# Optimization experiments

Measured on AMD Instinct MI355X. Metric: run time of the kernel, lower is better.

Reference implementation:

```python
import jax, jax.numpy as jnp
import numpy as np

N_NODES = 100000
N_EDGES = 1600000
D_IN = 512
D_HID = 128
N_CLASSES = 100


def _gcn_norm(edge_index, n_nodes):
    # Add self loops and compute symmetric normalization D^{-1/2} (A+I) D^{-1/2}
    sl = jnp.arange(n_nodes, dtype=edge_index.dtype)
    src = jnp.concatenate([edge_index[0], sl])
    dst = jnp.concatenate([edge_index[1], sl])
    deg = jax.ops.segment_sum(jnp.ones_like(dst, dtype=jnp.float32), dst,
                              num_segments=n_nodes)
    dinv = jnp.where(deg > 0, jax.lax.rsqrt(deg), 0.0)
    norm = dinv[src] * dinv[dst]  # [E + N]
    return src, dst, norm


def _gcn_layer(x, W, b, src, dst, norm, n_nodes):
    h = x @ W                                  # [N, d_out] (transform first, like PyG GCNConv)
    msg = h[src] * norm[:, None]               # [E+N, d_out] gather + scale
    out = jax.ops.segment_sum(msg, dst, num_segments=n_nodes)  # scatter-add
    return out + b


def setup_inputs() -> dict:
    key = jax.random.key(0)
    ks = jax.random.split(key, 6)
    x = jax.random.normal(ks[0], (N_NODES, D_IN), dtype=jnp.float32)
    edge_index = jax.random.randint(ks[1], (2, N_EDGES), 0, N_NODES, dtype=jnp.int64)
    W1 = jax.random.normal(ks[2], (D_IN, D_HID), dtype=jnp.float32) * (1.0 / np.sqrt(D_IN))
    b1 = jnp.zeros((D_HID,), dtype=jnp.float32)
    W2 = jax.random.normal(ks[3], (D_HID, N_CLASSES), dtype=jnp.float32) * (1.0 / np.sqrt(D_HID))
    b2 = jnp.zeros((N_CLASSES,), dtype=jnp.float32)
    return {"x": x, "edge_index": edge_index, "W1": W1, "b1": b1, "W2": W2, "b2": b2}


def reference(x, edge_index, W1, b1, W2, b2):
    n_nodes = x.shape[0]
    src, dst, norm = _gcn_norm(edge_index, n_nodes)
    h = jax.nn.relu(_gcn_layer(x, W1, b1, src, dst, norm, n_nodes))
    logits = _gcn_layer(h, W2, b2, src, dst, norm, n_nodes)
    return jax.nn.log_softmax(logits, axis=-1)
```

## Files before the change

### kernel.cpp

```cpp
#include <hip/hip_runtime.h>
#include <math.h>

typedef __attribute__((ext_vector_type(8))) short short8;
typedef __attribute__((ext_vector_type(4))) float f32x4;
typedef _Float16 half8 __attribute__((ext_vector_type(8)));
typedef __fp16 fp16x2 __attribute__((ext_vector_type(2)));
typedef unsigned int uint;

__device__ inline uint f2bf(float f) {
    uint u = __float_as_uint(f);
    return (u + 0x7fffu + ((u >> 16) & 1u)) >> 16;
}
__device__ inline uint pack2(float lo, float hi) { return f2bf(lo) | (f2bf(hi) << 16); }
__device__ inline float bflo(uint u) { return __uint_as_float(u << 16); }
__device__ inline float bfhi(uint u) { return __uint_as_float(u & 0xffff0000u); }
__device__ inline uint cvtpk(float lo, float hi) {
    uint r;
    asm("v_cvt_pk_bf16_f32 %0, %1, %2" : "=v"(r) : "v"(lo), "v"(hi));
    return r;
}
__device__ inline uint pkh(float lo, float hi) {
    union { fp16x2 h; uint u; } c;
    c.h = __builtin_amdgcn_cvt_pkrtz(lo, hi);
    return c.u;
}
__device__ inline void gload16(const void* g, void* l) {
    __builtin_amdgcn_global_load_lds(
        (const __attribute__((address_space(1))) void*)g,
        (__attribute__((address_space(3))) void*)l, 16, 0, 0);
}

__global__ void k_prep(const int* __restrict__ dst, int E, int nbE, int* __restrict__ cnt,
                       const float* __restrict__ W1, ushort* __restrict__ w1frag,
                       const float* __restrict__ W2, const float* __restrict__ b2,
                       ushort* __restrict__ w2frag, float* __restrict__ b2pad) {
    int bid = blockIdx.x;
    if (bid < nbE) {
        int i = bid * 256 + threadIdx.x;
        if (i < E) atomicAdd(&cnt[dst[i]], 1);
        return;
    }
    bid -= nbE;
    if (bid < 32) {
        int tid = bid * 256 + threadIdx.x;
        int ks = tid >> 9;
        int t = (tid >> 6) & 7;
        int l = tid & 63;
        int kbase = ks * 32 + (l >> 4) * 8;
        int c = t * 16 + (l & 15);
#pragma unroll
        for (int j = 0; j < 8; j++) {
            float v = W1[(size_t)(kbase + j) * 128 + c];
            union { _Float16 h; ushort u; } cv;
            cv.h = (_Float16)v;
            w1frag[(size_t)tid * 8 + j] = cv.u;
        }
        return;
    }
    bid -= 32;
    {
        int tid = bid * 256 + threadIdx.x;
        if (tid < 1792) {
            int q = tid / 448;
            int t = (tid >> 6) % 7;
            int l = tid & 63;
            int kbase = q * 32 + (l >> 4) * 8;
            int c = t * 16 + (l & 15);
#pragma unroll
            for (int j = 0; j < 8; j++) {
                float v = (c < 100) ? W2[(kbase + j) * 100 + c] : 0.f;
                w2frag[(size_t)tid * 8 + j] = (ushort)f2bf(v);
            }
        } else if (tid < 1792 + 112) {
            int c = tid - 1792;
            b2pad[c] = (c < 100) ? b2[c] : -1e30f;
        }
    }
}

__global__ __launch_bounds__(512) void k_scan1(const int* __restrict__ cnt, int* __restrict__ rp,
                                               int* __restrict__ partials, float* __restrict__ dinv,
                                               int N) {
    __shared__ int s[512];
    int i = blockIdx.x * 512 + threadIdx.x;
    int v = (i < N) ? cnt[i] : 0;
    if (i < N) dinv[i] = rsqrtf((float)(v + 1));
    s[threadIdx.x] = v;
    __syncthreads();
    for (int d = 1; d < 512; d <<= 1) {
        int t = (threadIdx.x >= d) ? s[threadIdx.x - d] : 0;
        __syncthreads();
        s[threadIdx.x] += t;
        __syncthreads();
    }
    if (i < N) rp[i] = s[threadIdx.x] - v;
    if (threadIdx.x == 511) partials[blockIdx.x] = s[511];
}

__global__ __launch_bounds__(256) void k_scan2(int* __restrict__ partials, int nb) {
    __shared__ int s[256];
    int carry = 0;
    for (int base = 0; base < nb; base += 256) {
        int i = base + threadIdx.x;
        int v = (i < nb) ? partials[i] : 0;
        s[threadIdx.x] = v;
        __syncthreads();
        for (int d = 1; d < 256; d <<= 1) {
            int t = (threadIdx.x >= d) ? s[threadIdx.x - d] : 0;
            __syncthreads();
            s[threadIdx.x] += t;
            __syncthreads();
        }
        if (i < nb) partials[i] = carry + s[threadIdx.x] - v;
        carry += s[255];
        __syncthreads();
    }
}

__global__ __launch_bounds__(512) void k_scan3(int* __restrict__ rp, const int* __restrict__ partials,
                                               int N, int E) {
    int i = blockIdx.x * 512 + threadIdx.x;
    if (i < N) rp[i] += partials[blockIdx.x];
    if (i == 0) rp[N] = E;
}

__global__ void k_fill(const int* __restrict__ src, const int* __restrict__ dst, int E,
                       const int* __restrict__ rp, int* __restrict__ cursor,
                       const float* __restrict__ dinv, float2* __restrict__ colw) {
    int i = blockIdx.x * 256 + threadIdx.x;
    if (i < E) {
        int d = dst[i];
        int s = src[i];
        int pos = rp[d] + atomicAdd(&cursor[d], 1);
        colw[pos] = make_float2(__int_as_float(s), dinv[s]);
    }
}

__global__ __launch_bounds__(256) void k_gemm1(const float* __restrict__ x,
                                               const uint4* __restrict__ w1f,
                                               uint* __restrict__ h1, int N) {
    __shared__ __align__(16) char lds[40960];
    int tid = threadIdx.x, wv = tid >> 6, l = tid & 63;
    int cl = l & 15, kg = l >> 4;
    int row0 = blockIdx.x * 32;
    int rhalf = wv & 1, chalf = wv >> 1;

    int xr = tid >> 3, xs = tid & 7;
    int xrg = row0 + xr; if (xrg >= N) xrg = N - 1;
    const float* xsrc = x + (size_t)xrg * 512 + xs * 8;

    auto stageB = [&](int c) {
        char* bbase = lds + 8192 + (c & 1) * 16384;
        const char* bsrc = (const char*)w1f + (size_t)c * 16384;
#pragma unroll
        for (int i = 0; i < 4; i++) {
            int s = i * 256 + tid;
            gload16(bsrc + (size_t)s * 16, bbase + (size_t)(s - l) * 16);
        }
    };

    float4 f0, f1;
    auto loadx = [&](int c) {
        const float* p = xsrc + c * 64;
        f0 = *(const float4*)p;
        f1 = *(const float4*)(p + 4);
    };
    auto writex = [&](int c) {
        char* xb = lds + (c & 1) * 4096;
        uint4 v;
        v.x = pkh(f0.x, f0.y);
        v.y = pkh(f0.z, f0.w);
        v.z = pkh(f1.x, f1.y);
        v.w = pkh(f1.z, f1.w);
        *(uint4*)(xb + xr * 128 + ((xs ^ (xr & 7)) * 16)) = v;
    };

    f32x4 acc[4];
#pragma unroll
    for (int t = 0; t < 4; t++) acc[t] = (f32x4){0.f, 0.f, 0.f, 0.f};

    union U { uint4 u4; half8 h8; };
    int arow = rhalf * 16 + cl;

    loadx(0);
    stageB(0);
    writex(0);
    __syncthreads();

    for (int c = 0; c < 8; c++) {
        if (c < 7) { loadx(c + 1); stageB(c + 1); }
        const char* xb = lds + (c & 1) * 4096;
        const char* bb = lds + 8192 + (c & 1) * 16384;
#pragma unroll
        for (int k2 = 0; k2 < 2; k2++) {
            U A;
            A.u4 = *(const uint4*)(xb + arow * 128 + (((k2 * 4 + kg) ^ (arow & 7)) * 16));
#pragma unroll
            for (int tt = 0; tt < 4; tt++) {
                U B;
                B.u4 = *(const uint4*)(bb + (size_t)(((k2 * 8 + chalf * 4 + tt) * 64 + l)) * 16);
                acc[tt] = __builtin_amdgcn_mfma_f32_16x16x32_f16(A.h8, B.h8, acc[tt], 0, 0, 0);
            }
        }
        if (c < 7) writex(c + 1);
        __syncthreads();
    }

    uint* hsp = (uint*)lds + (size_t)wv * (16 * 33);
#pragma unroll
    for (int tt = 0; tt < 4; tt++)
#pragma unroll
        for (int r = 0; r < 4; r++) {
            float mine = acc[tt][r];
            float other = __shfl_xor(mine, 1, 64);
            if ((cl & 1) == 0)
                hsp[(kg * 4 + r) * 33 + tt * 8 + (cl >> 1)] = cvtpk(mine, other);
        }
#pragma unroll
    for (int p = 0; p < 8; p++) {
        int it = p * 2 + (l >> 5);
        int gr = row0 + rhalf * 16 + it;
        if (gr < N) h1[(size_t)gr * 64 + chalf * 32 + (l & 31)] = hsp[it * 33 + (l & 31)];
    }
}

template <bool RELU_BIAS>
__global__ __launch_bounds__(256) void k_agg(const uint* __restrict__ h, const float* __restrict__ dinv,
                                             const int* __restrict__ rp, const float2* __restrict__ colw,
                                             const float* __restrict__ bias, uint* __restrict__ outb, int N) {
    int wave = threadIdx.x >> 6, lane = threadIdx.x & 63;
    int v = blockIdx.x * 4 + wave;
    if (v >= N) return;
    float dv = dinv[v];
    float wself = dv * dv;
    uint us = h[(size_t)v * 64 + lane];
    float acc0 = bflo(us) * wself;
    float acc1 = bfhi(us) * wself;
    int e0 = rp[v], e1 = rp[v + 1];
    int i = e0;
    for (; i + 8 <= e1; i += 8) {
        float2 q[8];
        uint u[8];
#pragma unroll
        for (int j = 0; j < 8; j++) q[j] = colw[i + j];
#pragma unroll
        for (int j = 0; j < 8; j++) u[j] = h[(size_t)__float_as_int(q[j].x) * 64 + lane];
#pragma unroll
        for (int j = 0; j < 8; j++) {
            float w = q[j].y * dv;
            acc0 = fmaf(bflo(u[j]), w, acc0);
            acc1 = fmaf(bfhi(u[j]), w, acc1);
        }
    }
    if (i + 4 <= e1) {
        float2 q[4];
        uint u[4];
#pragma unroll
        for (int j = 0; j < 4; j++) q[j] = colw[i + j];
#pragma unroll
        for (int j = 0; j < 4; j++) u[j] = h[(size_t)__float_as_int(q[j].x) * 64 + lane];
#pragma unroll
        for (int j = 0; j < 4; j++) {
            float w = q[j].y * dv;
            acc0 = fmaf(bflo(u[j]), w, acc0);
            acc1 = fmaf(bfhi(u[j]), w, acc1);
        }
        i += 4;
    }
    for (; i < e1; i++) {
        float2 q = colw[i];
        uint u = h[(size_t)__float_as_int(q.x) * 64 + lane];
        float w = q.y * dv;
        acc0 = fmaf(bflo(u), w, acc0);
        acc1 = fmaf(bfhi(u), w, acc1);
    }
    if (RELU_BIAS) {
        float2 b = *(const float2*)&bias[2 * lane];
        acc0 = fmaxf(acc0 + b.x, 0.f);
        acc1 = fmaxf(acc1 + b.y, 0.f);
    }
    outb[(size_t)v * 64 + lane] = pack2(acc0, acc1);
}

__global__ __launch_bounds__(256) void k_out_mfma(const uint* __restrict__ g2u,
                                                  const uint4* __restrict__ w2fragG,
                                                  const float* __restrict__ b2pad,
                                                  float* __restrict__ out, int N) {
    __shared__ uint4 w2s[1792];
    __shared__ float b2s[112];
    int tid = threadIdx.x;
    for (int i = tid; i < 1792; i += 256) w2s[i] = w2fragG[i];
    if (tid < 112) b2s[tid] = b2pad[tid];
    __syncthreads();

    int w = tid >> 6, l = tid & 63;
    int v0 = blockIdx.x * 128 + w * 32;
    int cl = l & 15, gq = l >> 4;

    f32x4 acc[2][7];
#pragma unroll
    for (int m = 0; m < 2; m++)
#pragma unroll
        for (int t = 0; t < 7; t++) acc[m][t] = (f32x4){0.f, 0.f, 0.f, 0.f};

    union U { uint4 u4; short8 s8; };

#pragma unroll
    for (int q = 0; q < 4; q++) {
        short8 afr[2];
#pragma unroll
        for (int m = 0; m < 2; m++) {
            int rv = v0 + m * 16 + cl;
            if (rv >= N) rv = N - 1;
            U a;
            a.u4 = *(const uint4*)&g2u[(size_t)rv * 64 + q * 16 + gq * 4];
            afr[m] = a.s8;
        }
#pragma unroll
        for (int t = 0; t < 7; t++) {
            U b;
            b.u4 = w2s[(q * 7 + t) * 64 + l];
            acc[0][t] = __builtin_amdgcn_mfma_f32_16x16x32_bf16(afr[0], b.s8, acc[0][t], 0, 0, 0);
            acc[1][t] = __builtin_amdgcn_mfma_f32_16x16x32_bf16(afr[1], b.s8, acc[1][t], 0, 0, 0);
        }
    }

    float bsv[7];
#pragma unroll
    for (int t = 0; t < 7; t++) bsv[t] = b2s[t * 16 + cl];

#pragma unroll
    for (int m = 0; m < 2; m++) {
#pragma unroll
        for (int r = 0; r < 4; r++) {
            int row = v0 + m * 16 + gq * 4 + r;
            float lg[7];
#pragma unroll
            for (int t = 0; t < 7; t++) lg[t] = acc[m][t][r] + bsv[t];
            float mx = lg[0];
#pragma unroll
            for (int t = 1; t < 7; t++) mx = fmaxf(mx, lg[t]);
            mx = fmaxf(mx, __shfl_xor(mx, 1, 64));
            mx = fmaxf(mx, __shfl_xor(mx, 2, 64));
            mx = fmaxf(mx, __shfl_xor(mx, 4, 64));
            mx = fmaxf(mx, __shfl_xor(mx, 8, 64));
            float s = 0.f;
#pragma unroll
            for (int t = 0; t < 7; t++) s += __expf(lg[t] - mx);
            s += __shfl_xor(s, 1, 64);
            s += __shfl_xor(s, 2, 64);
            s += __shfl_xor(s, 4, 64);
            s += __shfl_xor(s, 8, 64);
            float lse = mx + __logf(s);
            if (row < N) {
#pragma unroll
                for (int t = 0; t < 7; t++) {
                    int c = t * 16 + cl;
                    if (c < 100) out[(size_t)row * 100 + c] = lg[t] - lse;
                }
            }
        }
    }
}

extern "C" void kernel_launch(void* const* d_in, const int* in_sizes, int n_in,
                              void* d_out, int out_size, void* d_ws, size_t ws_size,
                              hipStream_t stream) {
    const float* x  = (const float*)d_in[0];
    const int*   ei = (const int*)d_in[1];
    const float* W1 = (const float*)d_in[2];
    const float* b1 = (const float*)d_in[3];
    const float* W2 = (const float*)d_in[4];
    const float* b2 = (const float*)d_in[5];
    float* out = (float*)d_out;

    int N = in_sizes[0] / 512;
    int E = in_sizes[1] / 2;
    const int* srcI = ei;
    const int* dstI = ei + E;

    char* wsb = (char*)d_ws;
    size_t off = 0;
    auto alloc = [&](size_t bytes) {
        void* p = wsb + off;
        off = (off + bytes + 255) & ~(size_t)255;
        return p;
    };
    int*    cnt      = (int*)alloc((size_t)N * 4);
    int*    cursor   = (int*)alloc((size_t)N * 4);
    float*  dinv     = (float*)alloc((size_t)N * 4);
    int*    rp       = (int*)alloc((size_t)(N + 1) * 4);
    int*    partials = (int*)alloc(1024 * 4);
    ushort* w1f      = (ushort*)alloc(8192 * 8 * 2);
    ushort* w2frag   = (ushort*)alloc(1792 * 8 * 2);
    float*  b2pad    = (float*)alloc(112 * 4);
    float2* colw     = (float2*)alloc((size_t)E * 8);
    uint*   h1       = (uint*)alloc((size_t)N * 64 * 4);
    uint*   a1       = (uint*)alloc((size_t)N * 64 * 4);
    uint*   g2       = h1;

    hipMemsetAsync(cnt, 0, (size_t)2 * (((size_t)N * 4 + 255) & ~(size_t)255), stream);

    int nbE = (E + 255) / 256;
    k_prep<<<nbE + 40, 256, 0, stream>>>(dstI, E, nbE, cnt, W1, w1f, W2, b2, w2frag, b2pad);
    int nb = (N + 511) / 512;
    k_scan1<<<nb, 512, 0, stream>>>(cnt, rp, partials, dinv, N);
    k_scan2<<<1, 256, 0, stream>>>(partials, nb);
    k_scan3<<<nb, 512, 0, stream>>>(rp, partials, N, E);
    k_fill<<<(E + 255) / 256, 256, 0, stream>>>(srcI, dstI, E, rp, cursor, dinv, colw);

    k_gemm1<<<(N + 31) / 32, 256, 0, stream>>>(x, (const uint4*)w1f, h1, N);
    k_agg<true><<<(N + 3) / 4, 256, 0, stream>>>(h1, dinv, rp, colw, b1, a1, N);
    k_agg<false><<<(N + 3) / 4, 256, 0, stream>>>(a1, dinv, rp, colw, nullptr, g2, N);
    k_out_mfma<<<(N + 127) / 128, 256, 0, stream>>>(g2, (const uint4*)w2frag, b2pad, out, N);
}
```

Baseline: 378.6 us.

## Fuse CSR build into one cooperative kernel and widen GEMM1 blocks

Replaces the memset, prep, three scan kernels and fill kernel with a single cooperative kernel that uses grid-wide syncs between the zeroing, count, scan, offset and fill phases. This removes several launch gaps and the memset. The GEMM1 kernel now uses 512-thread blocks covering 64 rows, so each staged W1 chunk is shared by more rows. The cost is grid.sync overhead, a fixed 1024-block grid doing strided loops, and larger LDS use per block, which may lower occupancy.

```diff
diff --git a/kernel.cpp b/kernel.cpp
--- a/kernel.cpp
+++ b/kernel.cpp
@@ -1,5 +1,8 @@
 #include <hip/hip_runtime.h>
+#include <hip/hip_cooperative_groups.h>
 #include <math.h>
+
+namespace cg = cooperative_groups;
 
 typedef __attribute__((ext_vector_type(8))) short short8;
 typedef __attribute__((ext_vector_type(4))) float f32x4;
@@ -30,131 +33,127 @@
         (__attribute__((address_space(3))) void*)l, 16, 0, 0);
 }
 
-__global__ void k_prep(const int* __restrict__ dst, int E, int nbE, int* __restrict__ cnt,
-                       const float* __restrict__ W1, ushort* __restrict__ w1frag,
-                       const float* __restrict__ W2, const float* __restrict__ b2,
-                       ushort* __restrict__ w2frag, float* __restrict__ b2pad) {
-    int bid = blockIdx.x;
-    if (bid < nbE) {
-        int i = bid * 256 + threadIdx.x;
-        if (i < E) atomicAdd(&cnt[dst[i]], 1);
-        return;
-    }
-    bid -= nbE;
-    if (bid < 32) {
-        int tid = bid * 256 + threadIdx.x;
-        int ks = tid >> 9;
-        int t = (tid >> 6) & 7;
-        int l = tid & 63;
+__global__ __launch_bounds__(256) void k_csr(const int* __restrict__ src, const int* __restrict__ dst,
+                                             int E, int N, int* __restrict__ cnt, int* __restrict__ cursor,
+                                             int* __restrict__ rp, int* __restrict__ tsum,
+                                             float* __restrict__ dinv, float2* __restrict__ colw,
+                                             const float* __restrict__ W1, ushort* __restrict__ w1frag,
+                                             const float* __restrict__ W2, const float* __restrict__ b2,
+                                             ushort* __restrict__ w2frag, float* __restrict__ b2pad) {
+    cg::grid_group grid = cg::this_grid();
+    int gsz = gridDim.x * 256;
+    int gtid = blockIdx.x * 256 + threadIdx.x;
+    __shared__ int s[256];
+
+    for (int i = gtid; i < N; i += gsz) { cnt[i] = 0; cursor[i] = 0; }
+    for (int t = gtid; t < 8192; t += gsz) {
+        int ks = t >> 9;
+        int tt = (t >> 6) & 7;
+        int l = t & 63;
         int kbase = ks * 32 + (l >> 4) * 8;
-        int c = t * 16 + (l & 15);
+        int c = tt * 16 + (l & 15);
 #pragma unroll
         for (int j = 0; j < 8; j++) {
             float v = W1[(size_t)(kbase + j) * 128 + c];
             union { _Float16 h; ushort u; } cv;
             cv.h = (_Float16)v;
-            w1frag[(size_t)tid * 8 + j] = cv.u;
-        }
-        return;
-    }
-    bid -= 32;
-    {
-        int tid = bid * 256 + threadIdx.x;
-        if (tid < 1792) {
-            int q = tid / 448;
-            int t = (tid >> 6) % 7;
-            int l = tid & 63;
+            w1frag[(size_t)t * 8 + j] = cv.u;
+        }
+    }
+    for (int t = gtid; t < 2048; t += gsz) {
+        if (t < 1792) {
+            int q = t / 448;
+            int tt = (t >> 6) % 7;
+            int l = t & 63;
             int kbase = q * 32 + (l >> 4) * 8;
-            int c = t * 16 + (l & 15);
+            int c = tt * 16 + (l & 15);
 #pragma unroll
             for (int j = 0; j < 8; j++) {
                 float v = (c < 100) ? W2[(kbase + j) * 100 + c] : 0.f;
-                w2frag[(size_t)tid * 8 + j] = (ushort)f2bf(v);
+                w2frag[(size_t)t * 8 + j] = (ushort)f2bf(v);
             }
-        } else if (tid < 1792 + 112) {
-            int c = tid - 1792;
+        } else if (t < 1792 + 112) {
+            int c = t - 1792;
             b2pad[c] = (c < 100) ? b2[c] : -1e30f;
         }
     }
-}
-
-__global__ __launch_bounds__(512) void k_scan1(const int* __restrict__ cnt, int* __restrict__ rp,
-                                               int* __restrict__ partials, float* __restrict__ dinv,
-                                               int N) {
-    __shared__ int s[512];
-    int i = blockIdx.x * 512 + threadIdx.x;
-    int v = (i < N) ? cnt[i] : 0;
-    if (i < N) dinv[i] = rsqrtf((float)(v + 1));
-    s[threadIdx.x] = v;
-    __syncthreads();
-    for (int d = 1; d < 512; d <<= 1) {
-        int t = (threadIdx.x >= d) ? s[threadIdx.x - d] : 0;
-        __syncthreads();
-        s[threadIdx.x] += t;
-        __syncthreads();
-    }
-    if (i < N) rp[i] = s[threadIdx.x] - v;
-    if (threadIdx.x == 511) partials[blockIdx.x] = s[511];
-}
-
-__global__ __launch_bounds__(256) void k_scan2(int* __restrict__ partials, int nb) {
-    __shared__ int s[256];
-    int carry = 0;
-    for (int base = 0; base < nb; base += 256) {
-        int i = base + threadIdx.x;
-        int v = (i < nb) ? partials[i] : 0;
+    grid.sync();
+
+    for (int i = gtid; i < E; i += gsz) atomicAdd(&cnt[dst[i]], 1);
+    grid.sync();
+
+    int ntiles = (N + 255) >> 8;
+    for (int t = blockIdx.x; t < ntiles; t += gridDim.x) {
+        int i = t * 256 + threadIdx.x;
+        int v = (i < N) ? cnt[i] : 0;
         s[threadIdx.x] = v;
         __syncthreads();
         for (int d = 1; d < 256; d <<= 1) {
-            int t = (threadIdx.x >= d) ? s[threadIdx.x - d] : 0;
+            int tv = (threadIdx.x >= d) ? s[threadIdx.x - d] : 0;
             __syncthreads();
-            s[threadIdx.x] += t;
+            s[threadIdx.x] += tv;
             __syncthreads();
         }
-        if (i < nb) partials[i] = carry + s[threadIdx.x] - v;
-        carry += s[255];
+        if (i < N) rp[i] = s[threadIdx.x] - v;
+        if (threadIdx.x == 255) tsum[t] = s[255];
         __syncthreads();
     }
-}
-
-__global__ __launch_bounds__(512) void k_scan3(int* __restrict__ rp, const int* __restrict__ partials,
-                                               int N, int E) {
-    int i = blockIdx.x * 512 + threadIdx.x;
-    if (i < N) rp[i] += partials[blockIdx.x];
-    if (i == 0) rp[N] = E;
-}
-
-__global__ void k_fill(const int* __restrict__ src, const int* __restrict__ dst, int E,
-                       const int* __restrict__ rp, int* __restrict__ cursor,
-                       const float* __restrict__ dinv, float2* __restrict__ colw) {
-    int i = blockIdx.x * 256 + threadIdx.x;
-    if (i < E) {
+    grid.sync();
+
+    if (blockIdx.x == 0) {
+        int carry = 0;
+        for (int base = 0; base < ntiles; base += 256) {
+            int i = base + threadIdx.x;
+            int v = (i < ntiles) ? tsum[i] : 0;
+            s[threadIdx.x] = v;
+            __syncthreads();
+            for (int d = 1; d < 256; d <<= 1) {
+                int tv = (threadIdx.x >= d) ? s[threadIdx.x - d] : 0;
+                __syncthreads();
+                s[threadIdx.x] += tv;
+                __syncthreads();
+            }
+            if (i < ntiles) tsum[i] = carry + s[threadIdx.x] - v;
+            carry += s[255];
+            __syncthreads();
+        }
+    }
+    grid.sync();
+
+    for (int i = gtid; i < N; i += gsz) {
+        rp[i] += tsum[i >> 8];
+        dinv[i] = rsqrtf((float)(cnt[i] + 1));
+    }
+    if (gtid == 0) rp[N] = E;
+    grid.sync();
+
+    for (int i = gtid; i < E; i += gsz) {
         int d = dst[i];
-        int s = src[i];
+        int sc = src[i];
         int pos = rp[d] + atomicAdd(&cursor[d], 1);
-        colw[pos] = make_float2(__int_as_float(s), dinv[s]);
-    }
-}
-
-__global__ __launch_bounds__(256) void k_gemm1(const float* __restrict__ x,
+        colw[pos] = make_float2(__int_as_float(sc), dinv[sc]);
+    }
+}
+
+__global__ __launch_bounds__(512) void k_gemm1(const float* __restrict__ x,
                                                const uint4* __restrict__ w1f,
                                                uint* __restrict__ h1, int N) {
-    __shared__ __align__(16) char lds[40960];
+    __shared__ __align__(16) char lds[49152];
     int tid = threadIdx.x, wv = tid >> 6, l = tid & 63;
     int cl = l & 15, kg = l >> 4;
-    int row0 = blockIdx.x * 32;
-    int rhalf = wv & 1, chalf = wv >> 1;
+    int row0 = blockIdx.x * 64;
+    int rq = wv & 3, chalf = wv >> 2;
 
     int xr = tid >> 3, xs = tid & 7;
     int xrg = row0 + xr; if (xrg >= N) xrg = N - 1;
     const float* xsrc = x + (size_t)xrg * 512 + xs * 8;
 
     auto stageB = [&](int c) {
-        char* bbase = lds + 8192 + (c & 1) * 16384;
+        char* bbase = lds + 16384 + (c & 1) * 16384;
         const char* bsrc = (const char*)w1f + (size_t)c * 16384;
 #pragma unroll
-        for (int i = 0; i < 4; i++) {
-            int s = i * 256 + tid;
+        for (int i = 0; i < 2; i++) {
+            int s = i * 512 + tid;
             gload16(bsrc + (size_t)s * 16, bbase + (size_t)(s - l) * 16);
         }
     };
@@ -166,7 +165,7 @@
         f1 = *(const float4*)(p + 4);
     };
     auto writex = [&](int c) {
-        char* xb = lds + (c & 1) * 4096;
+        char* xb = lds + (c & 1) * 8192;
         uint4 v;
         v.x = pkh(f0.x, f0.y);
         v.y = pkh(f0.z, f0.w);
@@ -180,7 +179,7 @@
     for (int t = 0; t < 4; t++) acc[t] = (f32x4){0.f, 0.f, 0.f, 0.f};
 
     union U { uint4 u4; half8 h8; };
-    int arow = rhalf * 16 + cl;
+    int arow = rq * 16 + cl;
 
     loadx(0);
     stageB(0);
@@ -189,8 +188,8 @@
 
     for (int c = 0; c < 8; c++) {
         if (c < 7) { loadx(c + 1); stageB(c + 1); }
-        const char* xb = lds + (c & 1) * 4096;
-        const char* bb = lds + 8192 + (c & 1) * 16384;
+        const char* xb = lds + (c & 1) * 8192;
+        const char* bb = lds + 16384 + (c & 1) * 16384;
 #pragma unroll
         for (int k2 = 0; k2 < 2; k2++) {
             U A;
@@ -219,7 +218,7 @@
 #pragma unroll
     for (int p = 0; p < 8; p++) {
         int it = p * 2 + (l >> 5);
-        int gr = row0 + rhalf * 16 + it;
+        int gr = row0 + rq * 16 + it;
         if (gr < N) h1[(size_t)gr * 64 + chalf * 32 + (l & 31)] = hsp[it * 33 + (l & 31)];
     }
 }
@@ -399,17 +398,13 @@
     uint*   a1       = (uint*)alloc((size_t)N * 64 * 4);
     uint*   g2       = h1;
 
-    hipMemsetAsync(cnt, 0, (size_t)2 * (((size_t)N * 4 + 255) & ~(size_t)255), stream);
-
-    int nbE = (E + 255) / 256;
-    k_prep<<<nbE + 40, 256, 0, stream>>>(dstI, E, nbE, cnt, W1, w1f, W2, b2, w2frag, b2pad);
-    int nb = (N + 511) / 512;
-    k_scan1<<<nb, 512, 0, stream>>>(cnt, rp, partials, dinv, N);
-    k_scan2<<<1, 256, 0, stream>>>(partials, nb);
-    k_scan3<<<nb, 512, 0, stream>>>(rp, partials, N, E);
-    k_fill<<<(E + 255) / 256, 256, 0, stream>>>(srcI, dstI, E, rp, cursor, dinv, colw);
-
-    k_gemm1<<<(N + 31) / 32, 256, 0, stream>>>(x, (const uint4*)w1f, h1, N);
+    void* args[] = {(void*)&srcI, (void*)&dstI, (void*)&E, (void*)&N,
+                    (void*)&cnt, (void*)&cursor, (void*)&rp, (void*)&partials,
+                    (void*)&dinv, (void*)&colw, (void*)&W1, (void*)&w1f,
+                    (void*)&W2, (void*)&b2, (void*)&w2frag, (void*)&b2pad};
+    hipLaunchCooperativeKernel((void*)k_csr, dim3(1024), dim3(256), args, 0, stream);
+
+    k_gemm1<<<(N + 63) / 64, 512, 0, stream>>>(x, (const uint4*)w1f, h1, N);
     k_agg<true><<<(N + 3) / 4, 256, 0, stream>>>(h1, dinv, rp, colw, b1, a1, N);
     k_agg<false><<<(N + 3) / 4, 256, 0, stream>>>(a1, dinv, rp, colw, nullptr, g2, N);
     k_out_mfma<<<(N + 127) / 128, 256, 0, stream>>>(g2, (const uint4*)w2frag, b2pad, out, N);
```

Result: slower. 840.2 us (+121.9%).
